# Kernel optimization log

Hardware: AMD Instinct MI355X
Metric: run time of the kernel (lower is better)

Reference implementation:

```python
import jax, jax.numpy as jnp
import numpy as np

BASIS_ORDER = 7  # basis_dim = 8 (Chebyshev T_0..T_7 of tanh(x))


def chebyshev_basis(x, order=BASIS_ORDER):
    """x: [batch, in] -> [batch, in, order+1] Chebyshev basis on tanh(x)."""
    xt = jnp.tanh(x)
    terms = [jnp.ones_like(xt), xt]
    for _ in range(2, order + 1):
        terms.append(2.0 * xt * terms[-1] - terms[-2])
    return jnp.stack(terms[: order + 1], axis=-1)


def setup_inputs() -> dict:
    key = jax.random.key(0)
    k1, k2, k3 = jax.random.split(key, 3)
    batch, in_f, out_f, K = 4096, 1024, 1024, BASIS_ORDER + 1
    x = jax.random.normal(k1, (batch, in_f), dtype=jnp.float32)
    # Kaiming-uniform-ish init scale
    bound = 1.0 / np.sqrt(in_f * K)
    weights = jax.random.uniform(k2, (out_f, in_f, K), dtype=jnp.float32,
                                 minval=-bound, maxval=bound)
    bias_param = jax.random.uniform(k3, (out_f,), dtype=jnp.float32,
                                    minval=-bound, maxval=bound)
    return {"x": x, "weights": weights, "bias_param": bias_param}


def reference(x, weights, bias_param):
    # basis: [b, i, k]; weights: [o, i, k] -> out[b, o] = sum_{i,k} basis*W
    basis = chebyshev_basis(x)  # [batch, in, K]
    out = jnp.einsum('bik,oik->bo', basis, weights)
    return out + bias_param
```

## Files before the change

kernel.cpp:

```cpp
#include <hip/hip_runtime.h>
#include <hip/hip_bf16.h>

#define MD 4096
#define ND 1024
#define KD 8192
#define IN_F 1024

typedef __bf16 bf16x8 __attribute__((ext_vector_type(8)));
typedef float f32x4 __attribute__((ext_vector_type(4)));

#define N_BASIS (MD * IN_F)
#define N_CONV ((ND * KD) / 8)

__global__ __launch_bounds__(256) void prep_kernel(
    const float* __restrict__ x, const float* __restrict__ w,
    __bf16* __restrict__ A, __bf16* __restrict__ B) {
  int i = blockIdx.x * blockDim.x + threadIdx.x;
  if (i < N_BASIS) {
    float t = tanhf(x[i]);
    float two_t = 2.0f * t;
    float T0 = 1.0f;
    float T1 = t;
    float T2 = two_t * T1 - T0;
    float T3 = two_t * T2 - T1;
    float T4 = two_t * T3 - T2;
    float T5 = two_t * T4 - T3;
    float T6 = two_t * T5 - T4;
    float T7 = two_t * T6 - T5;
    bf16x8 v;
    v[0] = (__bf16)T0; v[1] = (__bf16)T1; v[2] = (__bf16)T2; v[3] = (__bf16)T3;
    v[4] = (__bf16)T4; v[5] = (__bf16)T5; v[6] = (__bf16)T6; v[7] = (__bf16)T7;
    *(bf16x8*)(A + (size_t)i * 8) = v;
  } else if (i < N_BASIS + N_CONV) {
    int j = i - N_BASIS;
    const float4* p = (const float4*)(w + (size_t)j * 8);
    float4 a = p[0], b = p[1];
    bf16x8 v;
    v[0] = (__bf16)a.x; v[1] = (__bf16)a.y; v[2] = (__bf16)a.z; v[3] = (__bf16)a.w;
    v[4] = (__bf16)b.x; v[5] = (__bf16)b.y; v[6] = (__bf16)b.z; v[7] = (__bf16)b.w;
    *(bf16x8*)(B + (size_t)j * 8) = v;
  }
}

#define BM 64
#define BN 128
#define BK 64

__global__ __launch_bounds__(256) void gemm_bias(
    const __bf16* __restrict__ A, const __bf16* __restrict__ B,
    const float* __restrict__ bias, float* __restrict__ C) {
  __shared__ __align__(16) __bf16 As[BM * BK];
  __shared__ __align__(16) __bf16 Bs[BN * BK];

  const int tid = threadIdx.x;
  const int wave = tid >> 6;
  const int lane = tid & 63;
  const int n0 = blockIdx.x * BN;
  const int m0 = blockIdx.y * BM;
  const int wm = wave >> 1;
  const int wn = wave & 1;

  const int ar = lane >> 3;
  const int swz_col = ((lane & 7) ^ ar) * 8;
  const __bf16* gA = A + (size_t)(m0 + wave * 16 + ar) * KD + swz_col;
  const __bf16* gB = B + (size_t)(n0 + wave * 32 + ar) * KD + swz_col;
  const __bf16* lA = As + (wave * 16) * BK;
  const __bf16* lB = Bs + (wave * 32) * BK;

  f32x4 acc[2][4];
#pragma unroll
  for (int i = 0; i < 2; i++)
#pragma unroll
    for (int j = 0; j < 4; j++) acc[i][j] = (f32x4){0.f, 0.f, 0.f, 0.f};

  const int fr = lane & 15;
  const int fr7 = fr & 7;
  const int qk = lane >> 4;

  for (int kt = 0; kt < KD; kt += BK) {
#pragma unroll
    for (int j = 0; j < 2; j++)
      __builtin_amdgcn_global_load_lds(
          (const __attribute__((address_space(1))) void*)(gA + kt + (size_t)j * 8 * KD),
          (__attribute__((address_space(3))) void*)(lA + j * 8 * BK), 16, 0, 0);
#pragma unroll
    for (int j = 0; j < 4; j++)
      __builtin_amdgcn_global_load_lds(
          (const __attribute__((address_space(1))) void*)(gB + kt + (size_t)j * 8 * KD),
          (__attribute__((address_space(3))) void*)(lB + j * 8 * BK), 16, 0, 0);
    __syncthreads();

#pragma unroll
    for (int s = 0; s < 2; s++) {
      const int pa = ((s * 4 + qk) ^ fr7) * 8;
      bf16x8 af[2], bfr[4];
#pragma unroll
      for (int mi = 0; mi < 2; mi++)
        af[mi] = *(const bf16x8*)&As[(wm * 32 + mi * 16 + fr) * BK + pa];
#pragma unroll
      for (int ni = 0; ni < 4; ni++)
        bfr[ni] = *(const bf16x8*)&Bs[(wn * 64 + ni * 16 + fr) * BK + pa];
#pragma unroll
      for (int mi = 0; mi < 2; mi++)
#pragma unroll
        for (int ni = 0; ni < 4; ni++)
          acc[mi][ni] = __builtin_amdgcn_mfma_f32_16x16x32_bf16(
              af[mi], bfr[ni], acc[mi][ni], 0, 0, 0);
    }
    __syncthreads();
  }

  const int col0 = n0 + wn * 64;
  const int row0 = m0 + wm * 32 + (lane >> 4) * 4;
#pragma unroll
  for (int ni = 0; ni < 4; ni++) {
    int col = col0 + ni * 16 + (lane & 15);
    float bv = bias[col];
#pragma unroll
    for (int mi = 0; mi < 2; mi++) {
      int row = row0 + mi * 16;
#pragma unroll
      for (int r = 0; r < 4; r++)
        C[(size_t)(row + r) * ND + col] = acc[mi][ni][r] + bv;
    }
  }
}

extern "C" void kernel_launch(void* const* d_in, const int* in_sizes, int n_in,
                              void* d_out, int out_size, void* d_ws, size_t ws_size,
                              hipStream_t stream) {
  const float* x = (const float*)d_in[0];
  const float* w = (const float*)d_in[1];
  const float* bias = (const float*)d_in[2];
  float* out = (float*)d_out;

  __bf16* Abf = (__bf16*)d_ws;
  __bf16* Bbf = (__bf16*)((char*)d_ws + (size_t)MD * KD * 2);

  {
    int n = N_BASIS + N_CONV;
    prep_kernel<<<(n + 255) / 256, 256, 0, stream>>>(x, w, Abf, Bbf);
  }
  {
    dim3 grid(ND / BN, MD / BM);
    gemm_bias<<<grid, 256, 0, stream>>>(Abf, Bbf, bias, out);
  }
}
```

Measured before the change: 200.8 us.

## Fuse Chebyshev basis generation into GEMM A-tile load

Removes the materialized bf16 basis matrix (64 MB write plus repeated reads) and computes tanh and the Chebyshev terms on the fly from x inside the GEMM mainloop, writing them directly into swizzled LDS. tanh is replaced by a fast exp2/rcp formulation. The basis is now recomputed by every column block (8x redundancy) and the x load is only one iteration ahead, so VALU work and latency move into the GEMM loop.

```diff
diff --git a/kernel.cpp b/kernel.cpp
--- a/kernel.cpp
+++ b/kernel.cpp
@@ -9,45 +9,46 @@
 typedef __bf16 bf16x8 __attribute__((ext_vector_type(8)));
 typedef float f32x4 __attribute__((ext_vector_type(4)));
 
-#define N_BASIS (MD * IN_F)
 #define N_CONV ((ND * KD) / 8)
 
-__global__ __launch_bounds__(256) void prep_kernel(
-    const float* __restrict__ x, const float* __restrict__ w,
-    __bf16* __restrict__ A, __bf16* __restrict__ B) {
-  int i = blockIdx.x * blockDim.x + threadIdx.x;
-  if (i < N_BASIS) {
-    float t = tanhf(x[i]);
-    float two_t = 2.0f * t;
-    float T0 = 1.0f;
-    float T1 = t;
-    float T2 = two_t * T1 - T0;
-    float T3 = two_t * T2 - T1;
-    float T4 = two_t * T3 - T2;
-    float T5 = two_t * T4 - T3;
-    float T6 = two_t * T5 - T4;
-    float T7 = two_t * T6 - T5;
-    bf16x8 v;
-    v[0] = (__bf16)T0; v[1] = (__bf16)T1; v[2] = (__bf16)T2; v[3] = (__bf16)T3;
-    v[4] = (__bf16)T4; v[5] = (__bf16)T5; v[6] = (__bf16)T6; v[7] = (__bf16)T7;
-    *(bf16x8*)(A + (size_t)i * 8) = v;
-  } else if (i < N_BASIS + N_CONV) {
-    int j = i - N_BASIS;
-    const float4* p = (const float4*)(w + (size_t)j * 8);
-    float4 a = p[0], b = p[1];
-    bf16x8 v;
-    v[0] = (__bf16)a.x; v[1] = (__bf16)a.y; v[2] = (__bf16)a.z; v[3] = (__bf16)a.w;
-    v[4] = (__bf16)b.x; v[5] = (__bf16)b.y; v[6] = (__bf16)b.z; v[7] = (__bf16)b.w;
-    *(bf16x8*)(B + (size_t)j * 8) = v;
-  }
+__global__ __launch_bounds__(256) void conv_kernel(
+    const float* __restrict__ w, __bf16* __restrict__ B) {
+  int j = blockIdx.x * blockDim.x + threadIdx.x;
+  const float4* p = (const float4*)(w + (size_t)j * 8);
+  float4 a = p[0], b = p[1];
+  bf16x8 v;
+  v[0] = (__bf16)a.x; v[1] = (__bf16)a.y; v[2] = (__bf16)a.z; v[3] = (__bf16)a.w;
+  v[4] = (__bf16)b.x; v[5] = (__bf16)b.y; v[6] = (__bf16)b.z; v[7] = (__bf16)b.w;
+  *(bf16x8*)(B + (size_t)j * 8) = v;
 }
 
 #define BM 64
 #define BN 128
 #define BK 64
 
+__device__ __forceinline__ bf16x8 cheb8(float xs) {
+  float ax = __builtin_fabsf(xs);
+  float e = __builtin_amdgcn_exp2f(ax * 2.88539008177792681472f);
+  float r = __builtin_amdgcn_rcpf(e + 1.0f);
+  float t = 1.0f - 2.0f * r;
+  t = __builtin_copysignf(t, xs);
+  float two_t = 2.0f * t;
+  float T0 = 1.0f;
+  float T1 = t;
+  float T2 = two_t * T1 - T0;
+  float T3 = two_t * T2 - T1;
+  float T4 = two_t * T3 - T2;
+  float T5 = two_t * T4 - T3;
+  float T6 = two_t * T5 - T4;
+  float T7 = two_t * T6 - T5;
+  bf16x8 v;
+  v[0] = (__bf16)T0; v[1] = (__bf16)T1; v[2] = (__bf16)T2; v[3] = (__bf16)T3;
+  v[4] = (__bf16)T4; v[5] = (__bf16)T5; v[6] = (__bf16)T6; v[7] = (__bf16)T7;
+  return v;
+}
+
 __global__ __launch_bounds__(256) void gemm_bias(
-    const __bf16* __restrict__ A, const __bf16* __restrict__ B,
+    const float* __restrict__ x, const __bf16* __restrict__ B,
     const float* __restrict__ bias, float* __restrict__ C) {
   __shared__ __align__(16) __bf16 As[BM * BK];
   __shared__ __align__(16) __bf16 Bs[BN * BK];
@@ -62,10 +63,15 @@
 
   const int ar = lane >> 3;
   const int swz_col = ((lane & 7) ^ ar) * 8;
-  const __bf16* gA = A + (size_t)(m0 + wave * 16 + ar) * KD + swz_col;
   const __bf16* gB = B + (size_t)(n0 + wave * 32 + ar) * KD + swz_col;
-  const __bf16* lA = As + (wave * 16) * BK;
   const __bf16* lB = Bs + (wave * 32) * BK;
+
+  const int br = tid >> 2;
+  const int bg0 = (tid & 3) * 2;
+  const float* xrow = x + (size_t)(m0 + br) * IN_F + bg0;
+  const int sw = br & 7;
+  __bf16* aw0 = As + br * BK + ((bg0 ^ sw) * 8);
+  __bf16* aw1 = As + br * BK + (((bg0 + 1) ^ sw) * 8);
 
   f32x4 acc[2][4];
 #pragma unroll
@@ -77,17 +83,22 @@
   const int fr7 = fr & 7;
   const int qk = lane >> 4;
 
+  float2 xv = *(const float2*)(xrow);
+
   for (int kt = 0; kt < KD; kt += BK) {
-#pragma unroll
-    for (int j = 0; j < 2; j++)
-      __builtin_amdgcn_global_load_lds(
-          (const __attribute__((address_space(1))) void*)(gA + kt + (size_t)j * 8 * KD),
-          (__attribute__((address_space(3))) void*)(lA + j * 8 * BK), 16, 0, 0);
 #pragma unroll
     for (int j = 0; j < 4; j++)
       __builtin_amdgcn_global_load_lds(
           (const __attribute__((address_space(1))) void*)(gB + kt + (size_t)j * 8 * KD),
           (__attribute__((address_space(3))) void*)(lB + j * 8 * BK), 16, 0, 0);
+
+    bf16x8 v0 = cheb8(xv.x);
+    bf16x8 v1 = cheb8(xv.y);
+    *(bf16x8*)aw0 = v0;
+    *(bf16x8*)aw1 = v1;
+
+    if (kt + BK < KD) xv = *(const float2*)(xrow + ((kt + BK) >> 3));
+
     __syncthreads();
 
 #pragma unroll
@@ -134,15 +145,10 @@
   const float* bias = (const float*)d_in[2];
   float* out = (float*)d_out;
 
-  __bf16* Abf = (__bf16*)d_ws;
-  __bf16* Bbf = (__bf16*)((char*)d_ws + (size_t)MD * KD * 2);
+  __bf16* Bbf = (__bf16*)d_ws;
 
-  {
-    int n = N_BASIS + N_CONV;
-    prep_kernel<<<(n + 255) / 256, 256, 0, stream>>>(x, w, Abf, Bbf);
-  }
-  {
-    dim3 grid(ND / BN, MD / BM);
-    gemm_bias<<<grid, 256, 0, stream>>>(Abf, Bbf, bias, out);
-  }
+  conv_kernel<<<N_CONV / 256, 256, 0, stream>>>(w, Bbf);
+
+  dim3 grid(ND / BN, MD / BM);
+  gemm_bias<<<grid, 256, 0, stream>>>(x, Bbf, bias, out);
 }
```

Result: slower. 214.4 us (+6.8%).
